# Kernel tuning notes

Hardware: AMD Instinct MI355X
Metric: run time of the kernel (lower is better)

Reference implementation:

```python
import jax, jax.numpy as jnp
import numpy as np

B, L, C = 2, 4096, 512
H, K = 8, 64
D = C // H
MIN_WINDOW = 1.0
SCALE_POWER = 0.3


def _rmsnorm(x, w, eps=1e-6):
    var = jnp.mean(x * x, axis=-1, keepdims=True)
    return w * (x * jax.lax.rsqrt(var + eps))


def setup_inputs() -> dict:
    key = jax.random.key(0)
    ks = jax.random.split(key, 16)
    n = jax.random.normal
    hid = max(C // 4, 8)
    return {
        "x": n(ks[0], (B, L, C), jnp.float32),
        "window_w": n(ks[1], (H, C), jnp.float32) * 0.02,
        "window_b": n(ks[2], (H,), jnp.float32) * 0.02,
        "window_gamma": jnp.ones((H,), jnp.float32),
        "offset_w": n(ks[3], (H, C), jnp.float32) * 0.02,
        "offset_b": n(ks[4], (H,), jnp.float32) * 0.02,
        "offset_gamma": jnp.ones((H,), jnp.float32),
        "kernel_w": n(ks[5], (H * K, C), jnp.float32) * 0.02,
        "kernel_b": n(ks[6], (H * K,), jnp.float32) * 0.02,
        "kernel_gamma": jnp.ones((H * K,), jnp.float32),
        "v_w": n(ks[7], (C, C), jnp.float32) * 0.02,
        "v_b": n(ks[8], (C,), jnp.float32) * 0.02,
        "se_w1": n(ks[9], (hid, C), jnp.float32) * 0.02,
        "se_w2": n(ks[10], (C, hid), jnp.float32) * 0.02,
        "out_w": n(ks[11], (C, C), jnp.float32) * 0.02,
    }


def reference(x, window_w, window_b, window_gamma, offset_w, offset_b, offset_gamma,
              kernel_w, kernel_b, kernel_gamma, v_w, v_b, se_w1, se_w2, out_w):
    dt = x.dtype
    max_window = min(int(L ** SCALE_POWER), K)          # 12 for L=4096
    half_max = max_window // 2                           # 6
    max_offset = float(int(L ** SCALE_POWER))            # 12
    S = 2 * half_max + 1                                 # 13 offsets

    # per-position learned window size, center offset, kernel weights
    window_raw = jax.nn.sigmoid(_rmsnorm(x @ window_w.T + window_b, window_gamma))
    window_sizes = MIN_WINDOW + window_raw * (max_window - MIN_WINDOW)   # (B,L,H)
    half_win = jnp.maximum(window_sizes * 0.5, 0.5)
    center_off = jnp.tanh(_rmsnorm(x @ offset_w.T + offset_b, offset_gamma)) * max_offset  # (B,L,H)
    kernel = jax.nn.silu(_rmsnorm(x @ kernel_w.T + kernel_b, kernel_gamma)).reshape(B, L, H, K)
    v = (x @ v_w.T + v_b).reshape(B, L, H, D)

    s_offs = jnp.arange(-half_max, half_max + 1, dtype=dt)               # (S,)
    pos = jnp.arange(L, dtype=dt)

    # gaussian window weight from relative distance  (B,L,H,S)
    rel = jnp.abs(s_offs) / half_win[..., None]
    win_w = jnp.exp(-rel * rel)

    # interpolate projected kernel weights along K by rel distance
    norm_pos = jnp.clip(rel, 0.0, 1.0) * (K - 1)
    idx_f = jnp.clip(norm_pos.astype(jnp.int32), 0, K - 2)
    w_c = norm_pos - idx_f.astype(dt)
    k_f = jnp.take_along_axis(kernel, idx_f, axis=-1)
    k_c = jnp.take_along_axis(kernel, idx_f + 1, axis=-1)
    ker_w = jnp.maximum(k_f * (1.0 - w_c) + k_c * w_c, 0.0)

    # deformable fractional neighbor positions  (B,L,H,S)
    nb = pos[None, :, None, None] + center_off[..., None] + s_offs
    valid = ((nb >= 0) & (nb < L)).astype(dt)
    weight = (ker_w + 1.0) * win_w * valid
    wsum = jnp.sum(weight, axis=-1)                                      # (B,L,H)

    pc = jnp.clip(nb, 0.0, L - 1.001)
    pf = jnp.clip(jnp.floor(pc).astype(jnp.int32), 0, L - 1)
    pcl = jnp.minimum(pf + 1, L - 1)
    frac = (pc - pf.astype(dt)).transpose(0, 2, 1, 3)                    # (B,H,L,S)

    vh = v.transpose(0, 2, 1, 3)                                         # (B,H,L,D)

    def gather(idx):  # idx (B,L,H,S) -> (B,H,L,S,D)
        it = idx.transpose(0, 2, 1, 3).reshape(B, H, L * S)
        return jnp.take_along_axis(vh, it[..., None], axis=2).reshape(B, H, L, S, D)

    val = gather(pf) * (1.0 - frac)[..., None] + gather(pcl) * frac[..., None]
    out_h = jnp.einsum('blhs,bhlsd->blhd', weight, val)
    out_h = out_h / jnp.maximum(wsum, 1.0)[..., None]
    out = out_h.reshape(B, L, C)

    # squeeze-excite over channels
    scale = jax.nn.sigmoid(jax.nn.silu(jnp.mean(out, axis=1) @ se_w1.T) @ se_w2.T)
    out = out * scale[:, None, :]
    return jax.nn.silu(out @ out_w.T)
```

## Files before the change

kernel.cpp:

```cpp
#include <hip/hip_runtime.h>
#include <hip/hip_bf16.h>
#include <cstddef>
#include <cstdint>


typedef _Float16 f16x8 __attribute__((ext_vector_type(8)));
typedef float f32x4 __attribute__((ext_vector_type(4)));

#define AS1 __attribute__((address_space(1)))
#define AS3 __attribute__((address_space(3)))

__device__ __forceinline__ void gload_lds16(const ushort* g, ushort* l) {
  __builtin_amdgcn_global_load_lds((const AS1 uint32_t*)g, (AS3 uint32_t*)l, 16, 0, 0);
}
__device__ __forceinline__ ushort f2h(float x) {
  _Float16 h = (_Float16)x;
  return __builtin_bit_cast(ushort, h);
}
__device__ __forceinline__ float h2f(ushort u) {
  return (float)__builtin_bit_cast(_Float16, u);
}
__device__ __forceinline__ float readlane_f(float v, int l) {
  return __int_as_float(__builtin_amdgcn_readlane(__float_as_int(v), l));
}
__device__ __forceinline__ float sigm(float z) { return 1.f / (1.f + __expf(-z)); }

template<int MODE>
__global__ __launch_bounds__(256, 2) void gemm_mfma(
    const ushort* __restrict__ A, const ushort* __restrict__ B,
    const float* __restrict__ bk, const float* __restrict__ bv,
    ushort* __restrict__ Ck, ushort* __restrict__ Cv,
    float* __restrict__ Cf)
{
  __shared__ ushort smem[2 * 8192];
  const int t = threadIdx.x, wid = t >> 6, l = t & 63;

  const int bid = blockIdx.x;
  const int xcd = bid & 7, idx = bid >> 3;
  const int bx = (xcd << 3) | (idx & 7);
  const int by = idx >> 3;
  const int m0 = bx * 128, n0 = by * 128;

  const ushort* Bp = B;
  if (MODE == 1) Bp += (size_t)(m0 >> 12) << 18;

  const int swz = ((t & 7) ^ ((t >> 3) & 7)) * 8;
  const ushort* gsrc[8];
  uint32_t loff[8];
#pragma unroll
  for (int i = 0; i < 4; i++) {
    gsrc[i]     = A  + (size_t)(m0 + i * 32 + (t >> 3)) * 512 + swz;
    gsrc[4 + i] = Bp + (size_t)(n0 + i * 32 + (t >> 3)) * 512 + swz;
    loff[i]     = (i * 32 + wid * 8) * 64;
    loff[4 + i] = 8192 + (i * 32 + wid * 8) * 64;
  }

  f32x4 acc[4][4];
#pragma unroll
  for (int m = 0; m < 4; m++)
#pragma unroll
    for (int n = 0; n < 4; n++) acc[m][n] = (f32x4){0.f, 0.f, 0.f, 0.f};

  const int wr = wid >> 1, wc = wid & 1;
  const int fr = l & 15, fq = l >> 4;

  for (int k0 = 0; k0 < 512; k0 += 64) {
#pragma unroll
    for (int j = 0; j < 8; j++) {
      gload_lds16(gsrc[j], &smem[loff[j]]);
      gsrc[j] += 64;
    }
    __syncthreads();

    f16x8 af[4][2], bf[4][2];
#pragma unroll
    for (int m = 0; m < 4; m++)
#pragma unroll
      for (int ks = 0; ks < 2; ks++) {
        const int ko = 8 * ((ks * 4 + fq) ^ (fr & 7));
        af[m][ks] = *(const f16x8*)&smem[(wr * 64 + m * 16 + fr) * 64 + ko];
        bf[m][ks] = *(const f16x8*)&smem[8192 + (wc * 64 + m * 16 + fr) * 64 + ko];
      }
#pragma unroll
    for (int ks = 0; ks < 2; ks++)
#pragma unroll
      for (int m = 0; m < 4; m++)
#pragma unroll
        for (int n = 0; n < 4; n++)
          acc[m][n] = __builtin_amdgcn_mfma_f32_16x16x32_f16(af[m][ks], bf[n][ks], acc[m][n], 0, 0, 0);
    __syncthreads();
  }

  const int rbase = m0 + wr * 64 + (l >> 4) * 4;
  const int cbase = n0 + wc * 64 + (l & 15);
#pragma unroll
  for (int m = 0; m < 4; m++)
#pragma unroll
    for (int n = 0; n < 4; n++) {
      const int c = cbase + n * 16;
#pragma unroll
      for (int j = 0; j < 4; j++) {
        const int r = rbase + m * 16 + j;
        float v = acc[m][n][j];
        if (MODE == 0) {
          if (n0 < 512) Ck[(size_t)r * 512 + c]         = f2h(v + bk[c]);
          else          Cv[(size_t)r * 512 + (c - 512)] = f2h(v + bv[c - 512]);
        } else {
          Cf[(size_t)r * 512 + c] = v * sigm(v);
        }
      }
    }
}

__global__ __launch_bounds__(256) void winoff_kernel(
    const float* __restrict__ x,
    const float* __restrict__ window_w, const float* __restrict__ window_b,
    const float* __restrict__ window_g,
    const float* __restrict__ offset_w, const float* __restrict__ offset_b,
    const float* __restrict__ offset_g,
    float* __restrict__ halfwin, float* __restrict__ cenoff,
    ushort* __restrict__ xh,
    const float* __restrict__ kernel_w, const float* __restrict__ v_w,
    ushort* __restrict__ wkv_h)
{
  const int t = threadIdx.x;
  if (blockIdx.x >= 512) {
    for (int i = (blockIdx.x - 512) * 256 + t; i < 131072; i += 32768) {
      float4 v = (i < 65536) ? ((const float4*)kernel_w)[i]
                             : ((const float4*)v_w)[i - 65536];
      ushort4 o = {f2h(v.x), f2h(v.y), f2h(v.z), f2h(v.w)};
      ((ushort4*)wkv_h)[i] = o;
    }
    return;
  }
  __shared__ float wsm[16][512];
  {
    float4* dst = (float4*)&wsm[0][0];
    for (int i = t; i < 2048; i += 256)
      dst[i] = (i < 1024) ? ((const float4*)window_w)[i] : ((const float4*)offset_w)[i - 1024];
  }
  __syncthreads();
  const int wid = t >> 6, lane = t & 63;
  for (int it = 0; it < 4; it++) {
    const int row = blockIdx.x * 16 + it * 4 + wid;
    const float4* xr4 = (const float4*)(x + (size_t)row * 512);
    float4 a0 = xr4[lane * 2], a1 = xr4[lane * 2 + 1];
    ushort4 h0 = {f2h(a0.x), f2h(a0.y), f2h(a0.z), f2h(a0.w)};
    ushort4 h1 = {f2h(a1.x), f2h(a1.y), f2h(a1.z), f2h(a1.w)};
    ((ushort4*)(xh + (size_t)row * 512))[lane * 2]     = h0;
    ((ushort4*)(xh + (size_t)row * 512))[lane * 2 + 1] = h1;
    float s[16];
#pragma unroll
    for (int n = 0; n < 16; n++) {
      const float4* wr = (const float4*)&wsm[n][0];
      float4 w0 = wr[lane * 2], w1 = wr[lane * 2 + 1];
      float p = a0.x * w0.x + a0.y * w0.y + a0.z * w0.z + a0.w * w0.w
              + a1.x * w1.x + a1.y * w1.y + a1.z * w1.z + a1.w * w1.w;
#pragma unroll
      for (int off = 32; off >= 1; off >>= 1) p += __shfl_xor(p, off);
      s[n] = p;
    }
    float ssw = 0.f, sso = 0.f;
#pragma unroll
    for (int h = 0; h < 8; h++) {
      s[h]     += window_b[h]; ssw += s[h] * s[h];
      s[8 + h] += offset_b[h]; sso += s[8 + h] * s[8 + h];
    }
    float rw = rsqrtf(ssw * 0.125f + 1e-6f);
    float ro = rsqrtf(sso * 0.125f + 1e-6f);
    if (lane < 8) {
      float z = window_g[lane] * s[lane] * rw;
      halfwin[(size_t)row * 8 + lane] = fmaxf((1.0f + sigm(z) * 11.0f) * 0.5f, 0.5f);
    } else if (lane < 16) {
      int h = lane - 8;
      float z = offset_g[h] * s[8 + h] * ro;
      float th = 1.f - 2.f / (__expf(2.f * z) + 1.f);
      cenoff[(size_t)row * 8 + h] = th * 12.0f;
    }
  }
}

__global__ __launch_bounds__(512) void conv_row_kernel(
    const float* __restrict__ halfwin, const float* __restrict__ cenoff,
    const ushort* __restrict__ kact_h, const float* __restrict__ kernel_g,
    const ushort* __restrict__ v_h, ushort* __restrict__ oh_h)
{
  __shared__ float red[8];
  const int bid = blockIdx.x;
  const int row = ((bid & 7) << 10) | (bid >> 3);
  const int t = threadIdx.x, w = t >> 6, lane = t & 63;
  const int b = row >> 12, l = row & 4095;

  float kraw = h2f(kact_h[(size_t)row * 512 + t]);
  float ss = kraw * kraw;
#pragma unroll
  for (int off = 32; off >= 1; off >>= 1) ss += __shfl_xor(ss, off);
  if (lane == 0) red[w] = ss;
  __syncthreads();
  float tot = red[0] + red[1] + red[2] + red[3]
            + red[4] + red[5] + red[6] + red[7];
  float r = rsqrtf(tot * (1.f / 512.f) + 1e-6f);
  float a = kernel_g[t] * kraw * r;
  float kn_l = a * sigm(a);

  const int gw = row * 8 + w;
  const float hw = halfwin[gw];
  const float co = cenoff[gw];
  const ushort* vbase = v_h + ((size_t)b * 4096) * 512 + w * 64 + lane;

  const float soff = (float)(lane - 6);
  float rel  = fabsf(soff) / hw;
  float ww   = __expf(-rel * rel);
  float npos = fminf(rel, 1.f) * 63.f;
  int   idxk = min((int)npos, 62);
  float wc   = npos - (float)idxk;
  float kf = __shfl(kn_l, idxk);
  float kc = __shfl(kn_l, idxk + 1);
  float kw = fmaxf(kf * (1.f - wc) + kc * wc, 0.f);
  float nb = (float)l + co + soff;
  float wgt = (lane < 13 && nb >= 0.f && nb < 4096.f) ? (kw + 1.f) * ww : 0.f;
  float pc  = fminf(fmaxf(nb, 0.f), 4094.999f);
  int   pfv = (int)pc;
  float frv = pc - (float)pfv;

  float wsum = wgt;
#pragma unroll
  for (int off = 32; off >= 1; off >>= 1) wsum += __shfl_xor(wsum, off);

  const int base = __builtin_amdgcn_readlane(pfv, 0);
  const bool ok = (lane >= 13) || (pfv == base + lane);
  const bool fast = __all((int)ok) && (base + 13 <= 4095);

  float acc0 = 0.f, acc1 = 0.f;
  if (fast) {
    float wfr = wgt * frv;
    float w1f = wgt - wfr;
    float up  = __shfl_up(wfr, 1);
    float u = (lane < 13 ? w1f : 0.f) + ((lane >= 1 && lane <= 13) ? up : 0.f);
    const ushort* vr = vbase + (size_t)base * 512;
    float xv[14];
#pragma unroll
    for (int rr = 0; rr < 14; rr++) xv[rr] = h2f(vr[(size_t)rr * 512]);
#pragma unroll
    for (int rr = 0; rr < 14; rr += 2) {
      acc0 = fmaf(readlane_f(u, rr),     xv[rr],     acc0);
      acc1 = fmaf(readlane_f(u, rr + 1), xv[rr + 1], acc1);
    }
  } else {
#pragma unroll
    for (int si = 0; si < 13; si++) {
      const float w_s  = readlane_f(wgt, si);
      const float fr_s = readlane_f(frv, si);
      const int   pf_s = __builtin_amdgcn_readlane(pfv, si);
      const int   pcl  = min(pf_s + 1, 4095);
      float v0 = h2f(vbase[(size_t)pf_s * 512]);
      float v1 = h2f(vbase[(size_t)pcl * 512]);
      acc0 = fmaf(w_s, v0 + fr_s * (v1 - v0), acc0);
    }
  }

  float val = (acc0 + acc1) / fmaxf(wsum, 1.f);
  oh_h[(size_t)row * 512 + w * 64 + lane] = f2h(val);
}

__global__ __launch_bounds__(256) void colpart_kernel(
    const ushort* __restrict__ oh_h, float* __restrict__ partial)
{
  const int blk = blockIdx.x;
  const int g = (blk & 7) * 16 + (blk >> 3);
  const int t = threadIdx.x;
  const size_t base = (size_t)g * 64 * 512;
  float s0 = 0.f, s1 = 0.f;
  for (int i = 0; i < 64; i++) {
    uint u = *(const uint*)(oh_h + base + (size_t)i * 512 + t * 2);
    s0 += h2f((ushort)(u & 0xffffu));
    s1 += h2f((ushort)(u >> 16));
  }
  partial[(size_t)g * 512 + t * 2]     = s0;
  partial[(size_t)g * 512 + t * 2 + 1] = s1;
}

__global__ __launch_bounds__(256) void se_hid_kernel(
    const float* __restrict__ partial, const float* __restrict__ w1,
    float* __restrict__ hid_g)
{
  const int wid = threadIdx.x >> 6, lane = threadIdx.x & 63;
  const int g = blockIdx.x * 4 + wid;
  const int b2 = g >> 7, j = g & 127;
  float4 m0 = {0.f, 0.f, 0.f, 0.f}, m1 = {0.f, 0.f, 0.f, 0.f};
#pragma unroll 8
  for (int ch = 0; ch < 64; ch++) {
    const float4* pr = (const float4*)(partial + (size_t)(b2 * 64 + ch) * 512);
    float4 a0 = pr[lane * 2], a1 = pr[lane * 2 + 1];
    m0.x += a0.x; m0.y += a0.y; m0.z += a0.z; m0.w += a0.w;
    m1.x += a1.x; m1.y += a1.y; m1.z += a1.z; m1.w += a1.w;
  }
  float4 wv0 = ((const float4*)(w1 + (size_t)j * 512))[lane * 2];
  float4 wv1 = ((const float4*)(w1 + (size_t)j * 512))[lane * 2 + 1];
  float p = (wv0.x * m0.x + wv0.y * m0.y + wv0.z * m0.z + wv0.w * m0.w
           + wv1.x * m1.x + wv1.y * m1.y + wv1.z * m1.z + wv1.w * m1.w) * (1.f / 4096.f);
#pragma unroll
  for (int off = 32; off >= 1; off >>= 1) p += __shfl_xor(p, off);
  if (lane == 0) hid_g[g] = p * sigm(p);
}

__global__ __launch_bounds__(256) void se_scale_kernel(
    const float* __restrict__ hid_g, const float* __restrict__ w2,
    float* __restrict__ scalebuf)
{
  const int wid = threadIdx.x >> 6, lane = threadIdx.x & 63;
  const int g = blockIdx.x * 4 + wid;
  const int b3 = g >> 9, c = g & 511;
  float2 wv = ((const float2*)(w2 + (size_t)c * 128))[lane];
  float2 hv = ((const float2*)(hid_g + b3 * 128))[lane];
  float p = wv.x * hv.x + wv.y * hv.y;
#pragma unroll
  for (int off = 32; off >= 1; off >>= 1) p += __shfl_xor(p, off);
  if (lane == 0) scalebuf[g] = sigm(p);
}

__global__ __launch_bounds__(256) void scale_w_kernel(
    const float* __restrict__ out_w, const float* __restrict__ scalebuf,
    ushort* __restrict__ dst)
{
  const int i = blockIdx.x * 256 + threadIdx.x;
  const int b = i >> 16, iw = i & 65535, c4 = i & 127;
  float4 v = ((const float4*)out_w)[iw];
  float4 s = ((const float4*)scalebuf)[b * 128 + c4];
  ushort4 o = {f2h(v.x * s.x), f2h(v.y * s.y), f2h(v.z * s.z), f2h(v.w * s.w)};
  ((ushort4*)dst)[i] = o;
}

extern "C" void kernel_launch(void* const* d_in, const int* in_sizes, int n_in,
                              void* d_out, int out_size, void* d_ws, size_t ws_size,
                              hipStream_t stream) {
  const float* x        = (const float*)d_in[0];
  const float* window_w = (const float*)d_in[1];
  const float* window_b = (const float*)d_in[2];
  const float* window_g = (const float*)d_in[3];
  const float* offset_w = (const float*)d_in[4];
  const float* offset_b = (const float*)d_in[5];
  const float* offset_g = (const float*)d_in[6];
  const float* kernel_w = (const float*)d_in[7];
  const float* kernel_b = (const float*)d_in[8];
  const float* kernel_g = (const float*)d_in[9];
  const float* v_w      = (const float*)d_in[10];
  const float* v_b      = (const float*)d_in[11];
  const float* se_w1    = (const float*)d_in[12];
  const float* se_w2    = (const float*)d_in[13];
  const float* out_w    = (const float*)d_in[14];
  float* out = (float*)d_out;
  char* ws   = (char*)d_ws;

  const size_t BLC = (size_t)8192 * 512;
  float* halfwin  = (float*)ws;                       ws += 65536 * 4;
  float* cenoff   = (float*)ws;                       ws += 65536 * 4;
  float* partial  = (float*)ws;                       ws += 128 * 512 * 4;
  float* hid_g    = (float*)ws;                       ws += 256 * 4;
  float* scalebuf = (float*)ws;                       ws += 1024 * 4;
  ushort* xh      = (ushort*)ws;                      ws += BLC * 2;
  ushort* wkv_h   = (ushort*)ws;                      ws += 1024 * 512 * 2;
  ushort* kact_h  = (ushort*)ws;                      ws += BLC * 2;
  ushort* v_h     = (ushort*)ws;                      ws += BLC * 2;
  ushort* oh_h    = (ushort*)ws;                      ws += BLC * 2;
  ushort* ow_h    = (ushort*)ws;                      ws += 2 * 512 * 512 * 2;

  winoff_kernel<<<640, 256, 0, stream>>>(x, window_w, window_b, window_g,
                                         offset_w, offset_b, offset_g,
                                         halfwin, cenoff, xh,
                                         kernel_w, v_w, wkv_h);
  gemm_mfma<0><<<512, 256, 0, stream>>>(xh, wkv_h, kernel_b, v_b,
                                        kact_h, v_h, nullptr);
  conv_row_kernel<<<8192, 512, 0, stream>>>(halfwin, cenoff, kact_h, kernel_g,
                                            v_h, oh_h);
  colpart_kernel<<<128, 256, 0, stream>>>(oh_h, partial);
  se_hid_kernel<<<64, 256, 0, stream>>>(partial, se_w1, hid_g);
  se_scale_kernel<<<256, 256, 0, stream>>>(hid_g, se_w2, scalebuf);
  scale_w_kernel<<<512, 256, 0, stream>>>(out_w, scalebuf, ow_h);
  gemm_mfma<1><<<256, 256, 0, stream>>>(oh_h, ow_h, nullptr, nullptr,
                                        nullptr, nullptr, out);
}
```

Before: 83.52 us.

## Fuse SE channel scaling into output GEMM A-tile load, drop scale_w kernel

Removes the separate kernel that scaled out_w per batch into fp16. out_w is now converted to fp16 once in the prologue kernel, and the SE scale is stored as fp16. The final GEMM multiplies the activation tile by the scale vector while loading it into LDS, using register loads and stores instead of direct global-to-LDS loads. This saves one launch and a weight rewrite, but adds register-path loads and a multiply to the GEMM's A loads.

```diff
diff --git a/kernel.cpp b/kernel.cpp
--- a/kernel.cpp
+++ b/kernel.cpp
@@ -30,7 +30,7 @@
     const ushort* __restrict__ A, const ushort* __restrict__ B,
     const float* __restrict__ bk, const float* __restrict__ bv,
     ushort* __restrict__ Ck, ushort* __restrict__ Cv,
-    float* __restrict__ Cf)
+    float* __restrict__ Cf, const ushort* __restrict__ scale_h)
 {
   __shared__ ushort smem[2 * 8192];
   const int t = threadIdx.x, wid = t >> 6, l = t & 63;
@@ -41,19 +41,21 @@
   const int by = idx >> 3;
   const int m0 = bx * 128, n0 = by * 128;
 
-  const ushort* Bp = B;
-  if (MODE == 1) Bp += (size_t)(m0 >> 12) << 18;
-
   const int swz = ((t & 7) ^ ((t >> 3) & 7)) * 8;
   const ushort* gsrc[8];
+  const ushort* asrc[4];
+  const ushort* sptr = nullptr;
   uint32_t loff[8];
 #pragma unroll
   for (int i = 0; i < 4; i++) {
-    gsrc[i]     = A  + (size_t)(m0 + i * 32 + (t >> 3)) * 512 + swz;
-    gsrc[4 + i] = Bp + (size_t)(n0 + i * 32 + (t >> 3)) * 512 + swz;
     loff[i]     = (i * 32 + wid * 8) * 64;
     loff[4 + i] = 8192 + (i * 32 + wid * 8) * 64;
-  }
+    if (MODE == 0) gsrc[i] = A + (size_t)(m0 + i * 32 + (t >> 3)) * 512 + swz;
+    else           asrc[i] = A + (size_t)(m0 + i * 32 + (t >> 3)) * 512 + swz;
+    gsrc[4 + i] = B + (size_t)(n0 + i * 32 + (t >> 3)) * 512 + swz;
+  }
+  if (MODE == 1) sptr = scale_h + (size_t)(m0 >> 12) * 512 + swz;
+  const uint32_t awr = (uint32_t)((t >> 3) * 64 + (t & 7) * 8);
 
   f32x4 acc[4][4];
 #pragma unroll
@@ -65,10 +67,25 @@
   const int fr = l & 15, fq = l >> 4;
 
   for (int k0 = 0; k0 < 512; k0 += 64) {
-#pragma unroll
-    for (int j = 0; j < 8; j++) {
-      gload_lds16(gsrc[j], &smem[loff[j]]);
-      gsrc[j] += 64;
+    if constexpr (MODE == 1) {
+      f16x8 sv = *(const f16x8*)sptr; sptr += 64;
+#pragma unroll
+      for (int i = 0; i < 4; i++) {
+        f16x8 av = *(const f16x8*)asrc[i]; asrc[i] += 64;
+        f16x8 pv = av * sv;
+        *(f16x8*)&smem[i * 32 * 64 + awr] = pv;
+      }
+#pragma unroll
+      for (int i = 0; i < 4; i++) {
+        gload_lds16(gsrc[4 + i], &smem[loff[4 + i]]);
+        gsrc[4 + i] += 64;
+      }
+    } else {
+#pragma unroll
+      for (int j = 0; j < 8; j++) {
+        gload_lds16(gsrc[j], &smem[loff[j]]);
+        gsrc[j] += 64;
+      }
     }
     __syncthreads();
 
@@ -121,15 +138,19 @@
     float* __restrict__ halfwin, float* __restrict__ cenoff,
     ushort* __restrict__ xh,
     const float* __restrict__ kernel_w, const float* __restrict__ v_w,
-    ushort* __restrict__ wkv_h)
+    const float* __restrict__ out_w,
+    ushort* __restrict__ wkv_h, ushort* __restrict__ ow16)
 {
   const int t = threadIdx.x;
   if (blockIdx.x >= 512) {
-    for (int i = (blockIdx.x - 512) * 256 + t; i < 131072; i += 32768) {
-      float4 v = (i < 65536) ? ((const float4*)kernel_w)[i]
-                             : ((const float4*)v_w)[i - 65536];
+    for (int i = (blockIdx.x - 512) * 256 + t; i < 196608; i += 32768) {
+      float4 v;
+      if (i < 65536)       v = ((const float4*)kernel_w)[i];
+      else if (i < 131072) v = ((const float4*)v_w)[i - 65536];
+      else                 v = ((const float4*)out_w)[i - 131072];
       ushort4 o = {f2h(v.x), f2h(v.y), f2h(v.z), f2h(v.w)};
-      ((ushort4*)wkv_h)[i] = o;
+      if (i < 131072) ((ushort4*)wkv_h)[i] = o;
+      else            ((ushort4*)ow16)[i - 131072] = o;
     }
     return;
   }
@@ -306,7 +327,7 @@
 
 __global__ __launch_bounds__(256) void se_scale_kernel(
     const float* __restrict__ hid_g, const float* __restrict__ w2,
-    float* __restrict__ scalebuf)
+    ushort* __restrict__ scale_h)
 {
   const int wid = threadIdx.x >> 6, lane = threadIdx.x & 63;
   const int g = blockIdx.x * 4 + wid;
@@ -316,19 +337,7 @@
   float p = wv.x * hv.x + wv.y * hv.y;
 #pragma unroll
   for (int off = 32; off >= 1; off >>= 1) p += __shfl_xor(p, off);
-  if (lane == 0) scalebuf[g] = sigm(p);
-}
-
-__global__ __launch_bounds__(256) void scale_w_kernel(
-    const float* __restrict__ out_w, const float* __restrict__ scalebuf,
-    ushort* __restrict__ dst)
-{
-  const int i = blockIdx.x * 256 + threadIdx.x;
-  const int b = i >> 16, iw = i & 65535, c4 = i & 127;
-  float4 v = ((const float4*)out_w)[iw];
-  float4 s = ((const float4*)scalebuf)[b * 128 + c4];
-  ushort4 o = {f2h(v.x * s.x), f2h(v.y * s.y), f2h(v.z * s.z), f2h(v.w * s.w)};
-  ((ushort4*)dst)[i] = o;
+  if (lane == 0) scale_h[g] = f2h(sigm(p));
 }
 
 extern "C" void kernel_launch(void* const* d_in, const int* in_sizes, int n_in,
@@ -357,26 +366,26 @@
   float* cenoff   = (float*)ws;                       ws += 65536 * 4;
   float* partial  = (float*)ws;                       ws += 128 * 512 * 4;
   float* hid_g    = (float*)ws;                       ws += 256 * 4;
-  float* scalebuf = (float*)ws;                       ws += 1024 * 4;
+  ushort* scale_h = (ushort*)ws;                      ws += 1024 * 2;
   ushort* xh      = (ushort*)ws;                      ws += BLC * 2;
   ushort* wkv_h   = (ushort*)ws;                      ws += 1024 * 512 * 2;
+  ushort* ow16    = (ushort*)ws;                      ws += 512 * 512 * 2;
   ushort* kact_h  = (ushort*)ws;                      ws += BLC * 2;
   ushort* v_h     = (ushort*)ws;                      ws += BLC * 2;
   ushort* oh_h    = (ushort*)ws;                      ws += BLC * 2;
-  ushort* ow_h    = (ushort*)ws;                      ws += 2 * 512 * 512 * 2;
 
   winoff_kernel<<<640, 256, 0, stream>>>(x, window_w, window_b, window_g,
                                          offset_w, offset_b, offset_g,
                                          halfwin, cenoff, xh,
-                                         kernel_w, v_w, wkv_h);
+                                         kernel_w, v_w, out_w,
+                                         wkv_h, ow16);
   gemm_mfma<0><<<512, 256, 0, stream>>>(xh, wkv_h, kernel_b, v_b,
-                                        kact_h, v_h, nullptr);
+                                        kact_h, v_h, nullptr, nullptr);
   conv_row_kernel<<<8192, 512, 0, stream>>>(halfwin, cenoff, kact_h, kernel_g,
                                             v_h, oh_h);
   colpart_kernel<<<128, 256, 0, stream>>>(oh_h, partial);
   se_hid_kernel<<<64, 256, 0, stream>>>(partial, se_w1, hid_g);
-  se_scale_kernel<<<256, 256, 0, stream>>>(hid_g, se_w2, scalebuf);
-  scale_w_kernel<<<512, 256, 0, stream>>>(out_w, scalebuf, ow_h);
-  gemm_mfma<1><<<256, 256, 0, stream>>>(oh_h, ow_h, nullptr, nullptr,
-                                        nullptr, nullptr, out);
-}
+  se_scale_kernel<<<256, 256, 0, stream>>>(hid_g, se_w2, scale_h);
+  gemm_mfma<1><<<256, 256, 0, stream>>>(oh_h, ow16, nullptr, nullptr,
+                                        nullptr, nullptr, out, scale_h);
+}
```

After: 84.23 us. No clear change (+0.8%).
